# Kernel optimization log

Hardware: AMD Instinct MI355X
Metric: run time of the kernel (lower is better)

Reference implementation:

```python
import jax, jax.numpy as jnp
import numpy as np

N_NODES = 100000
N_EDGES = 1600000
IN_FEATS = 128
N_HIDDEN = 128
N_CLASSES = 47


def _glorot(key, shape):
    lim = float(np.sqrt(6.0 / (shape[0] + shape[1])))
    return jax.random.uniform(key, shape, jnp.float32, -lim, lim)


def setup_inputs() -> dict:
    key = jax.random.key(0)
    ks = jax.random.split(key, 9)
    x = jax.random.normal(ks[0], (N_NODES, IN_FEATS), jnp.float32)
    src = jax.random.randint(ks[1], (N_EDGES,), 0, N_NODES, jnp.int32)
    dst = jax.random.randint(ks[2], (N_EDGES,), 0, N_NODES, jnp.int32)
    return {
        "x": x,
        "W_self_0": _glorot(ks[3], (IN_FEATS, N_HIDDEN)),
        "W_neigh_0": _glorot(ks[4], (IN_FEATS, N_HIDDEN)),
        "W_self_1": _glorot(ks[5], (N_HIDDEN, N_HIDDEN)),
        "W_neigh_1": _glorot(ks[6], (N_HIDDEN, N_HIDDEN)),
        "W_self_2": _glorot(ks[7], (N_HIDDEN, N_CLASSES)),
        "W_neigh_2": _glorot(ks[8], (N_HIDDEN, N_CLASSES)),
        "src": src,
        "dst": dst,
    }


def _sage_layer(h, src, dst, W_self, W_neigh):
    # mean aggregation of in-neighbor features (DGL SAGEConv 'mean', no bias)
    neigh_sum = jax.ops.segment_sum(h[src], dst, num_segments=N_NODES)  # [N, d]
    deg = jax.ops.segment_sum(jnp.ones((src.shape[0],), h.dtype), dst,
                              num_segments=N_NODES)  # [N]
    h_neigh = neigh_sum / jnp.maximum(deg, 1.0)[:, None]
    return h @ W_self + h_neigh @ W_neigh


def reference(x, W_self_0, W_neigh_0, W_self_1, W_neigh_1, W_self_2, W_neigh_2,
              src, dst):
    h = _sage_layer(x, src, dst, W_self_0, W_neigh_0)
    h = jax.nn.relu(h)  # dropout is identity in eval/reference mode
    h = _sage_layer(h, src, dst, W_self_1, W_neigh_1)
    h = jax.nn.relu(h)
    h = _sage_layer(h, src, dst, W_self_2, W_neigh_2)
    return h
```

## Files before the change

### kernel.cpp

```cpp
#include <hip/hip_runtime.h>
#include <hip/hip_bf16.h>

#define NN 100000
#define NE 1600000
#define NBK 196

typedef __attribute__((ext_vector_type(8))) short bf16x8;
typedef __attribute__((ext_vector_type(4))) float f32x4;

__device__ __forceinline__ unsigned short f2bf(float x) {
    unsigned u = __float_as_uint(x);
    return (unsigned short)((u + 0x7fffu + ((u >> 16) & 1u)) >> 16);
}
__device__ __forceinline__ float bflo(unsigned v) { return __uint_as_float(v << 16); }
__device__ __forceinline__ float bfhi(unsigned v) { return __uint_as_float(v & 0xffff0000u); }

__global__ void cast_x(const float* __restrict__ x, unsigned short* __restrict__ h, int n) {
    int i = (blockIdx.x * blockDim.x + threadIdx.x) * 4;
    if (i >= n) return;
    float4 v = *(const float4*)(x + i);
    unsigned out0 = ((unsigned)f2bf(v.y) << 16) | f2bf(v.x);
    unsigned out1 = ((unsigned)f2bf(v.w) << 16) | f2bf(v.z);
    *(uint2*)(h + i) = make_uint2(out0, out1);
}

__global__ __launch_bounds__(256) void hist_buck(const int* __restrict__ dst, int* __restrict__ bhist) {
    __shared__ int h[NBK];
    int t = threadIdx.x;
    if (t < NBK) h[t] = 0;
    __syncthreads();
    int base = blockIdx.x * 4096;
#pragma unroll
    for (int i = 0; i < 16; ++i) {
        int e = base + t + i * 256;
        if (e < NE) atomicAdd(&h[dst[e] >> 9], 1);
    }
    __syncthreads();
    if (t < NBK && h[t]) atomicAdd(&bhist[t], h[t]);
}

__global__ void scan_buck(const int* __restrict__ bhist, int* __restrict__ bbase,
                          int* __restrict__ gcur, int* __restrict__ row_ptr) {
    __shared__ int s[256];
    int t = threadIdx.x;
    int v = (t < NBK) ? bhist[t] : 0;
    s[t] = v;
    __syncthreads();
    for (int off = 1; off < 256; off <<= 1) {
        int u = (t >= off) ? s[t - off] : 0;
        __syncthreads();
        s[t] += u;
        __syncthreads();
    }
    int ex = s[t] - v;
    if (t <= NBK) bbase[t] = ex;
    if (t < NBK) gcur[t * 16] = ex;
    if (t == 0) row_ptr[NN] = NE;
}

__global__ __launch_bounds__(256) void sort_scatter(const int* __restrict__ src,
                                                    const int* __restrict__ dst,
                                                    int* __restrict__ gcur,
                                                    unsigned* __restrict__ pairs) {
    __shared__ int bcnt[NBK], gbase[NBK], lcur[NBK];
    int t = threadIdx.x;
    if (t < NBK) { bcnt[t] = 0; lcur[t] = 0; }
    __syncthreads();
    int base = blockIdx.x * 4096;
#pragma unroll
    for (int i = 0; i < 16; ++i) {
        int e = base + t + i * 256;
        if (e < NE) atomicAdd(&bcnt[dst[e] >> 9], 1);
    }
    __syncthreads();
    if (t < NBK) gbase[t] = atomicAdd(&gcur[t * 16], bcnt[t]);
    __syncthreads();
#pragma unroll
    for (int i = 0; i < 16; ++i) {
        int e = base + t + i * 256;
        if (e < NE) {
            int d = dst[e];
            int b = d >> 9;
            int p = atomicAdd(&lcur[b], 1);
            pairs[gbase[b] + p] = ((unsigned)src[e] << 9) | (unsigned)(d & 511);
        }
    }
}

__global__ __launch_bounds__(512) void bucket_place(const unsigned* __restrict__ pairs,
                                                    const int* __restrict__ bbase,
                                                    int* __restrict__ row_ptr,
                                                    float* __restrict__ inv_deg,
                                                    int* __restrict__ csr) {
    __shared__ int hist[512], sc[512], cur[512];
    int b = blockIdx.x, t = threadIdx.x;
    hist[t] = 0;
    __syncthreads();
    int beg = bbase[b], end = bbase[b + 1];
    for (int i = beg + t; i < end; i += 512) atomicAdd(&hist[pairs[i] & 511u], 1);
    __syncthreads();
    int deg = hist[t];
    sc[t] = deg;
    __syncthreads();
    for (int off = 1; off < 512; off <<= 1) {
        int u = (t >= off) ? sc[t - off] : 0;
        __syncthreads();
        sc[t] += u;
        __syncthreads();
    }
    int ex = sc[t] - deg;
    int node = b * 512 + t;
    if (node < NN) {
        row_ptr[node] = beg + ex;
        inv_deg[node] = 1.0f / (float)max(deg, 1);
    }
    cur[t] = beg + ex;
    __syncthreads();
    for (int i = beg + t; i < end; i += 512) {
        unsigned p = pairs[i];
        int pos = atomicAdd(&cur[p & 511u], 1);
        csr[pos] = (int)(p >> 9);
    }
}

__global__ void pack_w(const float* __restrict__ Wself, const float* __restrict__ Wneigh,
                       unsigned short* __restrict__ wpack, int Ncols, int NF) {
    int idx = blockIdx.x * blockDim.x + threadIdx.x;
    int total = 8 * NF * 64 * 8;
    if (idx >= total) return;
    int j = idx & 7;
    int lane = (idx >> 3) & 63;
    int fid = idx >> 9;
    int nf = fid % NF;
    int kstep = fid / NF;
    int k = kstep * 32 + (lane >> 4) * 8 + j;
    int n = nf * 16 + (lane & 15);
    float v = 0.f;
    if (n < Ncols) v = (k < 128) ? Wself[k * Ncols + n] : Wneigh[(k - 128) * Ncols + n];
    wpack[idx] = f2bf(v);
}

__global__ void aggregate(const unsigned* __restrict__ h32, const int* __restrict__ csr,
                          const int* __restrict__ row_ptr, const float* __restrict__ inv_deg,
                          unsigned* __restrict__ agg32) {
    int lane = threadIdx.x & 63;
    int node = blockIdx.x * (blockDim.x >> 6) + (threadIdx.x >> 6);
    if (node >= NN) return;
    int beg = row_ptr[node], end = row_ptr[node + 1];
    float a0 = 0.f, a1 = 0.f, b0 = 0.f, b1 = 0.f;
    int e = beg;
    for (; e + 7 < end; e += 8) {
        int s0 = csr[e], s1 = csr[e + 1], s2 = csr[e + 2], s3 = csr[e + 3];
        int s4 = csr[e + 4], s5 = csr[e + 5], s6 = csr[e + 6], s7 = csr[e + 7];
        unsigned v0 = h32[s0 * 64 + lane];
        unsigned v1 = h32[s1 * 64 + lane];
        unsigned v2 = h32[s2 * 64 + lane];
        unsigned v3 = h32[s3 * 64 + lane];
        unsigned v4 = h32[s4 * 64 + lane];
        unsigned v5 = h32[s5 * 64 + lane];
        unsigned v6 = h32[s6 * 64 + lane];
        unsigned v7 = h32[s7 * 64 + lane];
        a0 += bflo(v0) + bflo(v1) + bflo(v2) + bflo(v3);
        a1 += bfhi(v0) + bfhi(v1) + bfhi(v2) + bfhi(v3);
        b0 += bflo(v4) + bflo(v5) + bflo(v6) + bflo(v7);
        b1 += bfhi(v4) + bfhi(v5) + bfhi(v6) + bfhi(v7);
    }
    for (; e + 3 < end; e += 4) {
        int s0 = csr[e], s1 = csr[e + 1], s2 = csr[e + 2], s3 = csr[e + 3];
        unsigned v0 = h32[s0 * 64 + lane];
        unsigned v1 = h32[s1 * 64 + lane];
        unsigned v2 = h32[s2 * 64 + lane];
        unsigned v3 = h32[s3 * 64 + lane];
        a0 += bflo(v0) + bflo(v1) + bflo(v2) + bflo(v3);
        a1 += bfhi(v0) + bfhi(v1) + bfhi(v2) + bfhi(v3);
    }
    for (; e < end; ++e) {
        unsigned v = h32[csr[e] * 64 + lane];
        a0 += bflo(v);
        a1 += bfhi(v);
    }
    a0 += b0; a1 += b1;
    float inv = inv_deg[node];
    a0 *= inv; a1 *= inv;
    agg32[node * 64 + lane] = ((unsigned)f2bf(a1) << 16) | f2bf(a0);
}

template <int NF, bool LAST>
__global__ __launch_bounds__(256) void gemm_k(const unsigned short* __restrict__ hA,
                                              const unsigned short* __restrict__ hAgg,
                                              const unsigned short* __restrict__ wpack,
                                              unsigned short* __restrict__ hOut,
                                              float* __restrict__ fOut) {
    int lane = threadIdx.x & 63;
    int wave = threadIdx.x >> 6;
    int aRow = blockIdx.x * 64 + wave * 16 + (lane & 15);
    int kgrp = (lane >> 4) * 8;

    f32x4 acc[NF];
#pragma unroll
    for (int f = 0; f < NF; ++f)
#pragma unroll
        for (int r = 0; r < 4; ++r) acc[f][r] = 0.f;

    bool inb = (aRow < NN);
#pragma unroll
    for (int half = 0; half < 2; ++half) {
        const unsigned short* A = half ? hAgg : hA;
#pragma unroll
        for (int ks = 0; ks < 4; ++ks) {
            bf16x8 afrag;
            if (inb) {
                afrag = *(const bf16x8*)(A + aRow * 128 + ks * 32 + kgrp);
            } else {
#pragma unroll
                for (int j = 0; j < 8; ++j) afrag[j] = 0;
            }
            int kstep = half * 4 + ks;
#pragma unroll
            for (int nf = 0; nf < NF; ++nf) {
                bf16x8 b = *(const bf16x8*)(wpack + (((kstep * NF + nf) * 64) + lane) * 8);
                acc[nf] = __builtin_amdgcn_mfma_f32_16x16x32_bf16(afrag, b, acc[nf], 0, 0, 0);
            }
        }
    }

    int col0 = lane & 15;
    int rBase = blockIdx.x * 64 + wave * 16 + (lane >> 4) * 4;
#pragma unroll
    for (int nf = 0; nf < NF; ++nf) {
        int col = nf * 16 + col0;
        if (LAST) {
            if (col < 47) {
#pragma unroll
                for (int r = 0; r < 4; ++r) {
                    int row = rBase + r;
                    if (row < NN) fOut[row * 47 + col] = acc[nf][r];
                }
            }
        } else {
#pragma unroll
            for (int r = 0; r < 4; ++r) {
                int row = rBase + r;
                if (row < NN) hOut[row * 128 + col] = f2bf(fmaxf(acc[nf][r], 0.f));
            }
        }
    }
}

static inline size_t alignup(size_t x) { return (x + 255) & ~(size_t)255; }

extern "C" void kernel_launch(void* const* d_in, const int* in_sizes, int n_in,
                              void* d_out, int out_size, void* d_ws, size_t ws_size,
                              hipStream_t stream) {
    const float* x   = (const float*)d_in[0];
    const float* Ws0 = (const float*)d_in[1];
    const float* Wn0 = (const float*)d_in[2];
    const float* Ws1 = (const float*)d_in[3];
    const float* Wn1 = (const float*)d_in[4];
    const float* Ws2 = (const float*)d_in[5];
    const float* Wn2 = (const float*)d_in[6];
    const int* src   = (const int*)d_in[7];
    const int* dst   = (const int*)d_in[8];
    float* out = (float*)d_out;

    char* w = (char*)d_ws;
    size_t off = 0;
    int* row_ptr   = (int*)(w + off);   off += alignup((NN + 1) * 4);
    int* bhist     = (int*)(w + off);   off += alignup(NBK * 4);
    int* bbase     = (int*)(w + off);   off += alignup((NBK + 1) * 4);
    int* gcur      = (int*)(w + off);   off += alignup((size_t)NBK * 16 * 4);
    float* inv_deg = (float*)(w + off); off += alignup(NN * 4);
    int* csr       = (int*)(w + off);   off += alignup((size_t)NE * 4);
    unsigned short* wp0 = (unsigned short*)(w + off); off += alignup(8 * 8 * 64 * 8 * 2);
    unsigned short* wp1 = (unsigned short*)(w + off); off += alignup(8 * 8 * 64 * 8 * 2);
    unsigned short* wp2 = (unsigned short*)(w + off); off += alignup(8 * 3 * 64 * 8 * 2);
    unsigned short* hA  = (unsigned short*)(w + off); off += alignup((size_t)NN * 128 * 2);
    unsigned short* hB  = (unsigned short*)(w + off); off += alignup((size_t)NN * 128 * 2);
    unsigned short* agg = (unsigned short*)(w + off); off += alignup((size_t)NN * 128 * 2);
    unsigned* pairs = (unsigned*)agg;

    hipMemsetAsync(bhist, 0, NBK * 4, stream);

    cast_x<<<dim3((NN * 128 / 4 + 255) / 256), dim3(256), 0, stream>>>(x, hA, NN * 128);
    hist_buck<<<dim3((NE + 4095) / 4096), dim3(256), 0, stream>>>(dst, bhist);
    scan_buck<<<dim3(1), dim3(256), 0, stream>>>(bhist, bbase, gcur, row_ptr);
    sort_scatter<<<dim3((NE + 4095) / 4096), dim3(256), 0, stream>>>(src, dst, gcur, pairs);
    bucket_place<<<dim3(NBK), dim3(512), 0, stream>>>(pairs, bbase, row_ptr, inv_deg, csr);

    pack_w<<<dim3((8 * 8 * 64 * 8 + 255) / 256), dim3(256), 0, stream>>>(Ws0, Wn0, wp0, 128, 8);
    pack_w<<<dim3((8 * 8 * 64 * 8 + 255) / 256), dim3(256), 0, stream>>>(Ws1, Wn1, wp1, 128, 8);
    pack_w<<<dim3((8 * 3 * 64 * 8 + 255) / 256), dim3(256), 0, stream>>>(Ws2, Wn2, wp2, 47, 3);

    const int gemmGrid = (NN + 63) / 64;

    aggregate<<<dim3(NN / 4), dim3(256), 0, stream>>>((const unsigned*)hA, csr, row_ptr, inv_deg, (unsigned*)agg);
    gemm_k<8, false><<<dim3(gemmGrid), dim3(256), 0, stream>>>(hA, agg, wp0, hB, nullptr);
    aggregate<<<dim3(NN / 4), dim3(256), 0, stream>>>((const unsigned*)hB, csr, row_ptr, inv_deg, (unsigned*)agg);
    gemm_k<8, false><<<dim3(gemmGrid), dim3(256), 0, stream>>>(hB, agg, wp1, hA, nullptr);
    aggregate<<<dim3(NN / 4), dim3(256), 0, stream>>>((const unsigned*)hA, csr, row_ptr, inv_deg, (unsigned*)agg);
    gemm_k<3, true><<<dim3(gemmGrid), dim3(256), 0, stream>>>(hA, agg, wp2, nullptr, out);
}
```

Before: 340.6 us.

## Fuse neighbor aggregation into GEMM via LDS-staged swizzled aggregate tile

```diff
diff --git a/kernel.cpp b/kernel.cpp
--- a/kernel.cpp
+++ b/kernel.cpp
@@ -119,7 +119,7 @@
     for (int i = beg + t; i < end; i += 512) {
         unsigned p = pairs[i];
         int pos = atomicAdd(&cur[p & 511u], 1);
-        csr[pos] = (int)(p >> 9);
+        csr[pos] = (int)(p >> 9) << 8;
     }
 }
 
@@ -140,108 +140,126 @@
     wpack[idx] = f2bf(v);
 }
 
-__global__ void aggregate(const unsigned* __restrict__ h32, const int* __restrict__ csr,
-                          const int* __restrict__ row_ptr, const float* __restrict__ inv_deg,
-                          unsigned* __restrict__ agg32) {
-    int lane = threadIdx.x & 63;
-    int node = blockIdx.x * (blockDim.x >> 6) + (threadIdx.x >> 6);
-    if (node >= NN) return;
-    int beg = row_ptr[node], end = row_ptr[node + 1];
-    float a0 = 0.f, a1 = 0.f, b0 = 0.f, b1 = 0.f;
-    int e = beg;
-    for (; e + 7 < end; e += 8) {
-        int s0 = csr[e], s1 = csr[e + 1], s2 = csr[e + 2], s3 = csr[e + 3];
-        int s4 = csr[e + 4], s5 = csr[e + 5], s6 = csr[e + 6], s7 = csr[e + 7];
-        unsigned v0 = h32[s0 * 64 + lane];
-        unsigned v1 = h32[s1 * 64 + lane];
-        unsigned v2 = h32[s2 * 64 + lane];
-        unsigned v3 = h32[s3 * 64 + lane];
-        unsigned v4 = h32[s4 * 64 + lane];
-        unsigned v5 = h32[s5 * 64 + lane];
-        unsigned v6 = h32[s6 * 64 + lane];
-        unsigned v7 = h32[s7 * 64 + lane];
-        a0 += bflo(v0) + bflo(v1) + bflo(v2) + bflo(v3);
-        a1 += bfhi(v0) + bfhi(v1) + bfhi(v2) + bfhi(v3);
-        b0 += bflo(v4) + bflo(v5) + bflo(v6) + bflo(v7);
-        b1 += bfhi(v4) + bfhi(v5) + bfhi(v6) + bfhi(v7);
-    }
-    for (; e + 3 < end; e += 4) {
-        int s0 = csr[e], s1 = csr[e + 1], s2 = csr[e + 2], s3 = csr[e + 3];
-        unsigned v0 = h32[s0 * 64 + lane];
-        unsigned v1 = h32[s1 * 64 + lane];
-        unsigned v2 = h32[s2 * 64 + lane];
-        unsigned v3 = h32[s3 * 64 + lane];
-        a0 += bflo(v0) + bflo(v1) + bflo(v2) + bflo(v3);
-        a1 += bfhi(v0) + bfhi(v1) + bfhi(v2) + bfhi(v3);
-    }
-    for (; e < end; ++e) {
-        unsigned v = h32[csr[e] * 64 + lane];
-        a0 += bflo(v);
-        a1 += bfhi(v);
-    }
-    a0 += b0; a1 += b1;
-    float inv = inv_deg[node];
-    a0 *= inv; a1 *= inv;
-    agg32[node * 64 + lane] = ((unsigned)f2bf(a1) << 16) | f2bf(a0);
-}
-
 template <int NF, bool LAST>
-__global__ __launch_bounds__(256) void gemm_k(const unsigned short* __restrict__ hA,
-                                              const unsigned short* __restrict__ hAgg,
-                                              const unsigned short* __restrict__ wpack,
-                                              unsigned short* __restrict__ hOut,
-                                              float* __restrict__ fOut) {
+__global__ __launch_bounds__(256) void sage_layer(const unsigned* __restrict__ h32,
+                                                  const int* __restrict__ csr,
+                                                  const int* __restrict__ row_ptr,
+                                                  const float* __restrict__ inv_deg,
+                                                  const unsigned short* __restrict__ wpack,
+                                                  unsigned short* __restrict__ hOut,
+                                                  float* __restrict__ fOut) {
+    __shared__ unsigned lds_agg[64 * 64];
     int lane = threadIdx.x & 63;
     int wave = threadIdx.x >> 6;
-    int aRow = blockIdx.x * 64 + wave * 16 + (lane & 15);
+    int base = blockIdx.x * 64;
+    const char* hb = (const char*)h32;
+    unsigned lane4 = (unsigned)lane * 4;
+
+    for (int i = 0; i < 16; ++i) {
+        int node = base + wave * 16 + i;
+        float a0 = 0.f, a1 = 0.f, b0 = 0.f, b1 = 0.f;
+        float inv = 0.f;
+        if (node < NN) {
+            int beg = row_ptr[node], end = row_ptr[node + 1];
+            inv = inv_deg[node];
+            int e = beg;
+            for (; e + 7 < end; e += 8) {
+                unsigned o0 = (unsigned)csr[e]     + lane4;
+                unsigned o1 = (unsigned)csr[e + 1] + lane4;
+                unsigned o2 = (unsigned)csr[e + 2] + lane4;
+                unsigned o3 = (unsigned)csr[e + 3] + lane4;
+                unsigned o4 = (unsigned)csr[e + 4] + lane4;
+                unsigned o5 = (unsigned)csr[e + 5] + lane4;
+                unsigned o6 = (unsigned)csr[e + 6] + lane4;
+                unsigned o7 = (unsigned)csr[e + 7] + lane4;
+                unsigned v0 = *(const unsigned*)(hb + o0);
+                unsigned v1 = *(const unsigned*)(hb + o1);
+                unsigned v2 = *(const unsigned*)(hb + o2);
+                unsigned v3 = *(const unsigned*)(hb + o3);
+                unsigned v4 = *(const unsigned*)(hb + o4);
+                unsigned v5 = *(const unsigned*)(hb + o5);
+                unsigned v6 = *(const unsigned*)(hb + o6);
+                unsigned v7 = *(const unsigned*)(hb + o7);
+                a0 += bflo(v0) + bflo(v1) + bflo(v2) + bflo(v3);
+                a1 += bfhi(v0) + bfhi(v1) + bfhi(v2) + bfhi(v3);
+                b0 += bflo(v4) + bflo(v5) + bflo(v6) + bflo(v7);
+                b1 += bfhi(v4) + bfhi(v5) + bfhi(v6) + bfhi(v7);
+            }
+            for (; e + 3 < end; e += 4) {
+                unsigned v0 = *(const unsigned*)(hb + (unsigned)csr[e]     + lane4);
+                unsigned v1 = *(const unsigned*)(hb + (unsigned)csr[e + 1] + lane4);
+                unsigned v2 = *(const unsigned*)(hb + (unsigned)csr[e + 2] + lane4);
+                unsigned v3 = *(const unsigned*)(hb + (unsigned)csr[e + 3] + lane4);
+                a0 += bflo(v0) + bflo(v1) + bflo(v2) + bflo(v3);
+                a1 += bfhi(v0) + bfhi(v1) + bfhi(v2) + bfhi(v3);
+            }
+            for (; e < end; ++e) {
+                unsigned v = *(const unsigned*)(hb + (unsigned)csr[e] + lane4);
+                a0 += bflo(v);
+                a1 += bfhi(v);
+            }
+            a0 = (a0 + b0) * inv;
+            a1 = (a1 + b1) * inv;
+        }
+        int r = wave * 16 + i;
+        lds_agg[r * 64 + (lane ^ ((r & 7) << 2))] = ((unsigned)f2bf(a1) << 16) | f2bf(a0);
+    }
+    __syncthreads();
+
+    int aRow = base + wave * 16 + (lane & 15);
     int kgrp = (lane >> 4) * 8;
+    int r = wave * 16 + (lane & 15);
+    int swz = (r & 7) << 2;
+    bool inb = (aRow < NN);
+    const unsigned short* hA = (const unsigned short*)h32;
 
     f32x4 acc[NF];
 #pragma unroll
     for (int f = 0; f < NF; ++f)
 #pragma unroll
-        for (int r = 0; r < 4; ++r) acc[f][r] = 0.f;
-
-    bool inb = (aRow < NN);
-#pragma unroll
-    for (int half = 0; half < 2; ++half) {
-        const unsigned short* A = half ? hAgg : hA;
-#pragma unroll
-        for (int ks = 0; ks < 4; ++ks) {
-            bf16x8 afrag;
-            if (inb) {
-                afrag = *(const bf16x8*)(A + aRow * 128 + ks * 32 + kgrp);
-            } else {
-#pragma unroll
-                for (int j = 0; j < 8; ++j) afrag[j] = 0;
-            }
-            int kstep = half * 4 + ks;
-#pragma unroll
-            for (int nf = 0; nf < NF; ++nf) {
-                bf16x8 b = *(const bf16x8*)(wpack + (((kstep * NF + nf) * 64) + lane) * 8);
-                acc[nf] = __builtin_amdgcn_mfma_f32_16x16x32_bf16(afrag, b, acc[nf], 0, 0, 0);
-            }
+        for (int q = 0; q < 4; ++q) acc[f][q] = 0.f;
+
+#pragma unroll
+    for (int ks = 0; ks < 4; ++ks) {
+        bf16x8 aSelf;
+        if (inb) {
+            aSelf = *(const bf16x8*)(hA + (size_t)aRow * 128 + ks * 32 + kgrp);
+        } else {
+#pragma unroll
+            for (int j = 0; j < 8; ++j) aSelf[j] = 0;
+        }
+#pragma unroll
+        for (int nf = 0; nf < NF; ++nf) {
+            bf16x8 b = *(const bf16x8*)(wpack + (((ks * NF + nf) * 64) + lane) * 8);
+            acc[nf] = __builtin_amdgcn_mfma_f32_16x16x32_bf16(aSelf, b, acc[nf], 0, 0, 0);
+        }
+        int d0 = ks * 16 + (lane >> 4) * 4;
+        bf16x8 aAgg = *(const bf16x8*)&lds_agg[r * 64 + (d0 ^ swz)];
+#pragma unroll
+        for (int nf = 0; nf < NF; ++nf) {
+            bf16x8 b = *(const bf16x8*)(wpack + ((((4 + ks) * NF + nf) * 64) + lane) * 8);
+            acc[nf] = __builtin_amdgcn_mfma_f32_16x16x32_bf16(aAgg, b, acc[nf], 0, 0, 0);
         }
     }
 
     int col0 = lane & 15;
-    int rBase = blockIdx.x * 64 + wave * 16 + (lane >> 4) * 4;
+    int rBase = base + wave * 16 + (lane >> 4) * 4;
 #pragma unroll
     for (int nf = 0; nf < NF; ++nf) {
         int col = nf * 16 + col0;
         if (LAST) {
             if (col < 47) {
 #pragma unroll
-                for (int r = 0; r < 4; ++r) {
-                    int row = rBase + r;
-                    if (row < NN) fOut[row * 47 + col] = acc[nf][r];
+                for (int q = 0; q < 4; ++q) {
+                    int row = rBase + q;
+                    if (row < NN) fOut[(size_t)row * 47 + col] = acc[nf][q];
                 }
             }
         } else {
 #pragma unroll
-            for (int r = 0; r < 4; ++r) {
-                int row = rBase + r;
-                if (row < NN) hOut[row * 128 + col] = f2bf(fmaxf(acc[nf][r], 0.f));
+            for (int q = 0; q < 4; ++q) {
+                int row = rBase + q;
+                if (row < NN) hOut[(size_t)row * 128 + col] = f2bf(fmaxf(acc[nf][q], 0.f));
             }
         }
     }
@@ -271,13 +289,12 @@
     int* gcur      = (int*)(w + off);   off += alignup((size_t)NBK * 16 * 4);
     float* inv_deg = (float*)(w + off); off += alignup(NN * 4);
     int* csr       = (int*)(w + off);   off += alignup((size_t)NE * 4);
+    unsigned* pairs = (unsigned*)(w + off); off += alignup((size_t)NE * 4);
     unsigned short* wp0 = (unsigned short*)(w + off); off += alignup(8 * 8 * 64 * 8 * 2);
     unsigned short* wp1 = (unsigned short*)(w + off); off += alignup(8 * 8 * 64 * 8 * 2);
     unsigned short* wp2 = (unsigned short*)(w + off); off += alignup(8 * 3 * 64 * 8 * 2);
     unsigned short* hA  = (unsigned short*)(w + off); off += alignup((size_t)NN * 128 * 2);
     unsigned short* hB  = (unsigned short*)(w + off); off += alignup((size_t)NN * 128 * 2);
-    unsigned short* agg = (unsigned short*)(w + off); off += alignup((size_t)NN * 128 * 2);
-    unsigned* pairs = (unsigned*)agg;
 
     hipMemsetAsync(bhist, 0, NBK * 4, stream);
 
@@ -291,12 +308,11 @@
     pack_w<<<dim3((8 * 8 * 64 * 8 + 255) / 256), dim3(256), 0, stream>>>(Ws1, Wn1, wp1, 128, 8);
     pack_w<<<dim3((8 * 3 * 64 * 8 + 255) / 256), dim3(256), 0, stream>>>(Ws2, Wn2, wp2, 47, 3);
 
-    const int gemmGrid = (NN + 63) / 64;
-
-    aggregate<<<dim3(NN / 4), dim3(256), 0, stream>>>((const unsigned*)hA, csr, row_ptr, inv_deg, (unsigned*)agg);
-    gemm_k<8, false><<<dim3(gemmGrid), dim3(256), 0, stream>>>(hA, agg, wp0, hB, nullptr);
-    aggregate<<<dim3(NN / 4), dim3(256), 0, stream>>>((const unsigned*)hB, csr, row_ptr, inv_deg, (unsigned*)agg);
-    gemm_k<8, false><<<dim3(gemmGrid), dim3(256), 0, stream>>>(hB, agg, wp1, hA, nullptr);
-    aggregate<<<dim3(NN / 4), dim3(256), 0, stream>>>((const unsigned*)hA, csr, row_ptr, inv_deg, (unsigned*)agg);
-    gemm_k<3, true><<<dim3(gemmGrid), dim3(256), 0, stream>>>(hA, agg, wp2, nullptr, out);
-}
+    const int grid = (NN + 63) / 64;
+    sage_layer<8, false><<<dim3(grid), dim3(256), 0, stream>>>(
+        (const unsigned*)hA, csr, row_ptr, inv_deg, wp0, hB, nullptr);
+    sage_layer<8, false><<<dim3(grid), dim3(256), 0, stream>>>(
+        (const unsigned*)hB, csr, row_ptr, inv_deg, wp1, hA, nullptr);
+    sage_layer<3, true><<<dim3(grid), dim3(256), 0, stream>>>(
+        (const unsigned*)hA, csr, row_ptr, inv_deg, wp2, nullptr, out);
+}
```

After: 388.2 us. +14.0%, slower.

## Reorder last layer to transform-then-aggregate and vectorize neighbor gathers

Applied to the files above, without the earlier changes.

```diff
diff --git a/kernel.cpp b/kernel.cpp
--- a/kernel.cpp
+++ b/kernel.cpp
@@ -14,6 +14,12 @@
 }
 __device__ __forceinline__ float bflo(unsigned v) { return __uint_as_float(v << 16); }
 __device__ __forceinline__ float bfhi(unsigned v) { return __uint_as_float(v & 0xffff0000u); }
+
+#define ACC8(v) do { \
+    acc[0] += bflo((v).x); acc[1] += bfhi((v).x); \
+    acc[2] += bflo((v).y); acc[3] += bfhi((v).y); \
+    acc[4] += bflo((v).z); acc[5] += bfhi((v).z); \
+    acc[6] += bflo((v).w); acc[7] += bfhi((v).w); } while (0)
 
 __global__ void cast_x(const float* __restrict__ x, unsigned short* __restrict__ h, int n) {
     int i = (blockIdx.x * blockDim.x + threadIdx.x) * 4;
@@ -119,7 +125,7 @@
     for (int i = beg + t; i < end; i += 512) {
         unsigned p = pairs[i];
         int pos = atomicAdd(&cur[p & 511u], 1);
-        csr[pos] = (int)(p >> 9);
+        csr[pos] = (int)(p >> 9) << 8;
     }
 }
 
@@ -140,57 +146,122 @@
     wpack[idx] = f2bf(v);
 }
 
-__global__ void aggregate(const unsigned* __restrict__ h32, const int* __restrict__ csr,
-                          const int* __restrict__ row_ptr, const float* __restrict__ inv_deg,
-                          unsigned* __restrict__ agg32) {
+__global__ __launch_bounds__(256) void aggregate(const unsigned* __restrict__ h32,
+                                                 const int* __restrict__ csr,
+                                                 const int* __restrict__ row_ptr,
+                                                 const float* __restrict__ inv_deg,
+                                                 unsigned* __restrict__ agg32) {
     int lane = threadIdx.x & 63;
-    int node = blockIdx.x * (blockDim.x >> 6) + (threadIdx.x >> 6);
+    int wave = threadIdx.x >> 6;
+    int node = blockIdx.x * 4 + wave;
     if (node >= NN) return;
+    int g = lane >> 4;
+    unsigned l16 = (unsigned)(lane & 15) * 16;
+    const char* hb = (const char*)h32;
     int beg = row_ptr[node], end = row_ptr[node + 1];
-    float a0 = 0.f, a1 = 0.f, b0 = 0.f, b1 = 0.f;
+    float acc[8];
+#pragma unroll
+    for (int j = 0; j < 8; ++j) acc[j] = 0.f;
+
     int e = beg;
+    for (; e + 15 < end; e += 16) {
+        int c0 = csr[e + g];
+        int c1 = csr[e + 4 + g];
+        int c2 = csr[e + 8 + g];
+        int c3 = csr[e + 12 + g];
+        uint4 v0 = *(const uint4*)(hb + (unsigned)c0 + l16);
+        uint4 v1 = *(const uint4*)(hb + (unsigned)c1 + l16);
+        uint4 v2 = *(const uint4*)(hb + (unsigned)c2 + l16);
+        uint4 v3 = *(const uint4*)(hb + (unsigned)c3 + l16);
+        ACC8(v0); ACC8(v1); ACC8(v2); ACC8(v3);
+    }
+    for (; e + 3 < end; e += 4) {
+        int c = csr[e + g];
+        uint4 v = *(const uint4*)(hb + (unsigned)c + l16);
+        ACC8(v);
+    }
+    int rem = end - e;
+    if (g < rem) {
+        int c = csr[e + g];
+        uint4 v = *(const uint4*)(hb + (unsigned)c + l16);
+        ACC8(v);
+    }
+
+#pragma unroll
+    for (int j = 0; j < 8; ++j) {
+        acc[j] += __shfl_xor(acc[j], 16, 64);
+        acc[j] += __shfl_xor(acc[j], 32, 64);
+    }
+    float inv = inv_deg[node];
+    if (lane < 16) {
+        unsigned d0 = ((unsigned)f2bf(acc[1] * inv) << 16) | f2bf(acc[0] * inv);
+        unsigned d1 = ((unsigned)f2bf(acc[3] * inv) << 16) | f2bf(acc[2] * inv);
+        unsigned d2 = ((unsigned)f2bf(acc[5] * inv) << 16) | f2bf(acc[4] * inv);
+        unsigned d3 = ((unsigned)f2bf(acc[7] * inv) << 16) | f2bf(acc[6] * inv);
+        *(uint4*)((char*)agg32 + (size_t)node * 256 + l16) = make_uint4(d0, d1, d2, d3);
+    }
+}
+
+__global__ __launch_bounds__(256) void agg_out(const unsigned* __restrict__ g32,
+                                               const int* __restrict__ csr,
+                                               const int* __restrict__ row_ptr,
+                                               const float* __restrict__ inv_deg,
+                                               float* __restrict__ out) {
+    int lane = threadIdx.x & 63;
+    int wave = threadIdx.x >> 6;
+    int node = blockIdx.x * 4 + wave;
+    if (node >= NN) return;
+    int g = lane >> 3;
+    int l = lane & 7;
+    unsigned l16 = (unsigned)l * 16;
+    const char* gb = (const char*)g32;
+    int beg = row_ptr[node], end = row_ptr[node + 1];
+    float acc[8];
+#pragma unroll
+    for (int j = 0; j < 8; ++j) acc[j] = 0.f;
+
+    int e = beg;
+    for (; e + 15 < end; e += 16) {
+        int c0 = csr[e + g];
+        int c1 = csr[e + 8 + g];
+        uint4 v0 = *(const uint4*)(gb + ((unsigned)c0 >> 1) + l16);
+        uint4 v1 = *(const uint4*)(gb + ((unsigned)c1 >> 1) + l16);
+        ACC8(v0); ACC8(v1);
+    }
     for (; e + 7 < end; e += 8) {
-        int s0 = csr[e], s1 = csr[e + 1], s2 = csr[e + 2], s3 = csr[e + 3];
-        int s4 = csr[e + 4], s5 = csr[e + 5], s6 = csr[e + 6], s7 = csr[e + 7];
-        unsigned v0 = h32[s0 * 64 + lane];
-        unsigned v1 = h32[s1 * 64 + lane];
-        unsigned v2 = h32[s2 * 64 + lane];
-        unsigned v3 = h32[s3 * 64 + lane];
-        unsigned v4 = h32[s4 * 64 + lane];
-        unsigned v5 = h32[s5 * 64 + lane];
-        unsigned v6 = h32[s6 * 64 + lane];
-        unsigned v7 = h32[s7 * 64 + lane];
-        a0 += bflo(v0) + bflo(v1) + bflo(v2) + bflo(v3);
-        a1 += bfhi(v0) + bfhi(v1) + bfhi(v2) + bfhi(v3);
-        b0 += bflo(v4) + bflo(v5) + bflo(v6) + bflo(v7);
-        b1 += bfhi(v4) + bfhi(v5) + bfhi(v6) + bfhi(v7);
-    }
-    for (; e + 3 < end; e += 4) {
-        int s0 = csr[e], s1 = csr[e + 1], s2 = csr[e + 2], s3 = csr[e + 3];
-        unsigned v0 = h32[s0 * 64 + lane];
-        unsigned v1 = h32[s1 * 64 + lane];
-        unsigned v2 = h32[s2 * 64 + lane];
-        unsigned v3 = h32[s3 * 64 + lane];
-        a0 += bflo(v0) + bflo(v1) + bflo(v2) + bflo(v3);
-        a1 += bfhi(v0) + bfhi(v1) + bfhi(v2) + bfhi(v3);
-    }
-    for (; e < end; ++e) {
-        unsigned v = h32[csr[e] * 64 + lane];
-        a0 += bflo(v);
-        a1 += bfhi(v);
-    }
-    a0 += b0; a1 += b1;
+        int c = csr[e + g];
+        uint4 v = *(const uint4*)(gb + ((unsigned)c >> 1) + l16);
+        ACC8(v);
+    }
+    int rem = end - e;
+    if (g < rem) {
+        int c = csr[e + g];
+        uint4 v = *(const uint4*)(gb + ((unsigned)c >> 1) + l16);
+        ACC8(v);
+    }
+
+#pragma unroll
+    for (int j = 0; j < 8; ++j) {
+        acc[j] += __shfl_xor(acc[j], 8, 64);
+        acc[j] += __shfl_xor(acc[j], 16, 64);
+        acc[j] += __shfl_xor(acc[j], 32, 64);
+    }
     float inv = inv_deg[node];
-    a0 *= inv; a1 *= inv;
-    agg32[node * 64 + lane] = ((unsigned)f2bf(a1) << 16) | f2bf(a0);
-}
-
-template <int NF, bool LAST>
+    if (lane < 8) {
+        float* orow = out + (size_t)node * 47;
+#pragma unroll
+        for (int j = 0; j < 8; ++j) {
+            int f = l * 8 + j;
+            if (f < 47) orow[f] += acc[j] * inv;
+        }
+    }
+}
+
+template <int NF>
 __global__ __launch_bounds__(256) void gemm_k(const unsigned short* __restrict__ hA,
                                               const unsigned short* __restrict__ hAgg,
                                               const unsigned short* __restrict__ wpack,
-                                              unsigned short* __restrict__ hOut,
-                                              float* __restrict__ fOut) {
+                                              unsigned short* __restrict__ hOut) {
     int lane = threadIdx.x & 63;
     int wave = threadIdx.x >> 6;
     int aRow = blockIdx.x * 64 + wave * 16 + (lane & 15);
@@ -200,7 +271,7 @@
 #pragma unroll
     for (int f = 0; f < NF; ++f)
 #pragma unroll
-        for (int r = 0; r < 4; ++r) acc[f][r] = 0.f;
+        for (int q = 0; q < 4; ++q) acc[f][q] = 0.f;
 
     bool inb = (aRow < NN);
 #pragma unroll
@@ -210,7 +281,7 @@
         for (int ks = 0; ks < 4; ++ks) {
             bf16x8 afrag;
             if (inb) {
-                afrag = *(const bf16x8*)(A + aRow * 128 + ks * 32 + kgrp);
+                afrag = *(const bf16x8*)(A + (size_t)aRow * 128 + ks * 32 + kgrp);
             } else {
 #pragma unroll
                 for (int j = 0; j < 8; ++j) afrag[j] = 0;
@@ -229,19 +300,59 @@
 #pragma unroll
     for (int nf = 0; nf < NF; ++nf) {
         int col = nf * 16 + col0;
-        if (LAST) {
-            if (col < 47) {
-#pragma unroll
-                for (int r = 0; r < 4; ++r) {
-                    int row = rBase + r;
-                    if (row < NN) fOut[row * 47 + col] = acc[nf][r];
-                }
-            }
+#pragma unroll
+        for (int q = 0; q < 4; ++q) {
+            int row = rBase + q;
+            if (row < NN) hOut[(size_t)row * 128 + col] = f2bf(fmaxf(acc[nf][q], 0.f));
+        }
+    }
+}
+
+__global__ __launch_bounds__(256) void gemm_last(const unsigned short* __restrict__ hA,
+                                                 const unsigned short* __restrict__ wpack,
+                                                 unsigned short* __restrict__ g64,
+                                                 float* __restrict__ out) {
+    int lane = threadIdx.x & 63;
+    int wave = threadIdx.x >> 6;
+    int aRow = blockIdx.x * 64 + wave * 16 + (lane & 15);
+    int kgrp = (lane >> 4) * 8;
+
+    f32x4 accS[3], accG[3];
+#pragma unroll
+    for (int f = 0; f < 3; ++f)
+#pragma unroll
+        for (int q = 0; q < 4; ++q) { accS[f][q] = 0.f; accG[f][q] = 0.f; }
+
+    bool inb = (aRow < NN);
+#pragma unroll
+    for (int ks = 0; ks < 4; ++ks) {
+        bf16x8 afrag;
+        if (inb) {
+            afrag = *(const bf16x8*)(hA + (size_t)aRow * 128 + ks * 32 + kgrp);
         } else {
 #pragma unroll
-            for (int r = 0; r < 4; ++r) {
-                int row = rBase + r;
-                if (row < NN) hOut[row * 128 + col] = f2bf(fmaxf(acc[nf][r], 0.f));
+            for (int j = 0; j < 8; ++j) afrag[j] = 0;
+        }
+#pragma unroll
+        for (int nf = 0; nf < 3; ++nf) {
+            bf16x8 bS = *(const bf16x8*)(wpack + (((ks * 3 + nf) * 64) + lane) * 8);
+            accS[nf] = __builtin_amdgcn_mfma_f32_16x16x32_bf16(afrag, bS, accS[nf], 0, 0, 0);
+            bf16x8 bG = *(const bf16x8*)(wpack + ((((4 + ks) * 3 + nf) * 64) + lane) * 8);
+            accG[nf] = __builtin_amdgcn_mfma_f32_16x16x32_bf16(afrag, bG, accG[nf], 0, 0, 0);
+        }
+    }
+
+    int col0 = lane & 15;
+    int rBase = blockIdx.x * 64 + wave * 16 + (lane >> 4) * 4;
+#pragma unroll
+    for (int nf = 0; nf < 3; ++nf) {
+        int col = nf * 16 + col0;
+#pragma unroll
+        for (int q = 0; q < 4; ++q) {
+            int row = rBase + q;
+            if (row < NN) {
+                if (col < 47) out[(size_t)row * 47 + col] = accS[nf][q];
+                g64[(size_t)row * 64 + col] = f2bf(accG[nf][q]);
             }
         }
     }
@@ -271,13 +382,14 @@
     int* gcur      = (int*)(w + off);   off += alignup((size_t)NBK * 16 * 4);
     float* inv_deg = (float*)(w + off); off += alignup(NN * 4);
     int* csr       = (int*)(w + off);   off += alignup((size_t)NE * 4);
+    unsigned* pairs = (unsigned*)(w + off); off += alignup((size_t)NE * 4);
     unsigned short* wp0 = (unsigned short*)(w + off); off += alignup(8 * 8 * 64 * 8 * 2);
     unsigned short* wp1 = (unsigned short*)(w + off); off += alignup(8 * 8 * 64 * 8 * 2);
     unsigned short* wp2 = (unsigned short*)(w + off); off += alignup(8 * 3 * 64 * 8 * 2);
     unsigned short* hA  = (unsigned short*)(w + off); off += alignup((size_t)NN * 128 * 2);
     unsigned short* hB  = (unsigned short*)(w + off); off += alignup((size_t)NN * 128 * 2);
     unsigned short* agg = (unsigned short*)(w + off); off += alignup((size_t)NN * 128 * 2);
-    unsigned* pairs = (unsigned*)agg;
+    unsigned short* g64 = agg;
 
     hipMemsetAsync(bhist, 0, NBK * 4, stream);
 
@@ -291,12 +403,13 @@
     pack_w<<<dim3((8 * 8 * 64 * 8 + 255) / 256), dim3(256), 0, stream>>>(Ws1, Wn1, wp1, 128, 8);
     pack_w<<<dim3((8 * 3 * 64 * 8 + 255) / 256), dim3(256), 0, stream>>>(Ws2, Wn2, wp2, 47, 3);
 
+    const int aggGrid  = (NN + 3) / 4;
     const int gemmGrid = (NN + 63) / 64;
 
-    aggregate<<<dim3(NN / 4), dim3(256), 0, stream>>>((const unsigned*)hA, csr, row_ptr, inv_deg, (unsigned*)agg);
-    gemm_k<8, false><<<dim3(gemmGrid), dim3(256), 0, stream>>>(hA, agg, wp0, hB, nullptr);
-    aggregate<<<dim3(NN / 4), dim3(256), 0, stream>>>((const unsigned*)hB, csr, row_ptr, inv_deg, (unsigned*)agg);
-    gemm_k<8, false><<<dim3(gemmGrid), dim3(256), 0, stream>>>(hB, agg, wp1, hA, nullptr);
-    aggregate<<<dim3(NN / 4), dim3(256), 0, stream>>>((const unsigned*)hA, csr, row_ptr, inv_deg, (unsigned*)agg);
-    gemm_k<3, true><<<dim3(gemmGrid), dim3(256), 0, stream>>>(hA, agg, wp2, nullptr, out);
-}
+    aggregate<<<dim3(aggGrid), dim3(256), 0, stream>>>((const unsigned*)hA, csr, row_ptr, inv_deg, (unsigned*)agg);
+    gemm_k<8><<<dim3(gemmGrid), dim3(256), 0, stream>>>(hA, agg, wp0, hB);
+    aggregate<<<dim3(aggGrid), dim3(256), 0, stream>>>((const unsigned*)hB, csr, row_ptr, inv_deg, (unsigned*)agg);
+    gemm_k<8><<<dim3(gemmGrid), dim3(256), 0, stream>>>(hB, agg, wp1, hA);
+    gemm_last<<<dim3(gemmGrid), dim3(256), 0, stream>>>(hA, wp2, g64, out);
+    agg_out<<<dim3(aggGrid), dim3(256), 0, stream>>>((const unsigned*)g64, csr, row_ptr, inv_deg, out);
+}
```

Result: no change. 343.0 us (+0.7%).

## Restructure aggregation: two nodes per wave with 16-byte row gathers

Applied to the files above, without the earlier changes.

```diff
diff --git a/kernel.cpp b/kernel.cpp
--- a/kernel.cpp
+++ b/kernel.cpp
@@ -14,6 +14,31 @@
 }
 __device__ __forceinline__ float bflo(unsigned v) { return __uint_as_float(v << 16); }
 __device__ __forceinline__ float bfhi(unsigned v) { return __uint_as_float(v & 0xffff0000u); }
+
+#define ACCV(A, v) do { \
+    A[0] += bflo((v).x); A[1] += bfhi((v).x); \
+    A[2] += bflo((v).y); A[3] += bfhi((v).y); \
+    A[4] += bflo((v).z); A[5] += bfhi((v).z); \
+    A[6] += bflo((v).w); A[7] += bfhi((v).w); } while (0)
+
+#define DRAIN(A, e, end) do { \
+    for (; e + 15 < end; e += 16) { \
+        int c0 = csr[e + g], c1 = csr[e + 4 + g], c2 = csr[e + 8 + g], c3 = csr[e + 12 + g]; \
+        uint4 w0 = *(const uint4*)(hb + (unsigned)c0 + l16); \
+        uint4 w1 = *(const uint4*)(hb + (unsigned)c1 + l16); \
+        uint4 w2 = *(const uint4*)(hb + (unsigned)c2 + l16); \
+        uint4 w3 = *(const uint4*)(hb + (unsigned)c3 + l16); \
+        ACCV(A, w0); ACCV(A, w1); ACCV(A, w2); ACCV(A, w3); } \
+    for (; e + 3 < end; e += 4) { \
+        int c = csr[e + g]; \
+        uint4 w = *(const uint4*)(hb + (unsigned)c + l16); \
+        ACCV(A, w); } \
+    { int rem = end - e; \
+      if (g < rem) { \
+        int c = csr[e + g]; \
+        uint4 w = *(const uint4*)(hb + (unsigned)c + l16); \
+        ACCV(A, w); } } \
+} while (0)
 
 __global__ void cast_x(const float* __restrict__ x, unsigned short* __restrict__ h, int n) {
     int i = (blockIdx.x * blockDim.x + threadIdx.x) * 4;
@@ -119,70 +144,93 @@
     for (int i = beg + t; i < end; i += 512) {
         unsigned p = pairs[i];
         int pos = atomicAdd(&cur[p & 511u], 1);
-        csr[pos] = (int)(p >> 9);
-    }
-}
-
-__global__ void pack_w(const float* __restrict__ Wself, const float* __restrict__ Wneigh,
-                       unsigned short* __restrict__ wpack, int Ncols, int NF) {
+        csr[pos] = (int)(p >> 9) << 8;
+    }
+}
+
+__global__ void pack_w_all(const float* __restrict__ Ws0, const float* __restrict__ Wn0,
+                           const float* __restrict__ Ws1, const float* __restrict__ Wn1,
+                           const float* __restrict__ Ws2, const float* __restrict__ Wn2,
+                           unsigned short* __restrict__ wp0, unsigned short* __restrict__ wp1,
+                           unsigned short* __restrict__ wp2) {
     int idx = blockIdx.x * blockDim.x + threadIdx.x;
-    int total = 8 * NF * 64 * 8;
-    if (idx >= total) return;
-    int j = idx & 7;
-    int lane = (idx >> 3) & 63;
-    int fid = idx >> 9;
+    const float *Ws, *Wn;
+    unsigned short* wp;
+    int Ncols, NF, local;
+    if (idx < 32768)       { Ws = Ws0; Wn = Wn0; wp = wp0; Ncols = 128; NF = 8; local = idx; }
+    else if (idx < 65536)  { Ws = Ws1; Wn = Wn1; wp = wp1; Ncols = 128; NF = 8; local = idx - 32768; }
+    else if (idx < 77824)  { Ws = Ws2; Wn = Wn2; wp = wp2; Ncols = 47;  NF = 3; local = idx - 65536; }
+    else return;
+    int j = local & 7;
+    int lane = (local >> 3) & 63;
+    int fid = local >> 9;
     int nf = fid % NF;
     int kstep = fid / NF;
     int k = kstep * 32 + (lane >> 4) * 8 + j;
     int n = nf * 16 + (lane & 15);
     float v = 0.f;
-    if (n < Ncols) v = (k < 128) ? Wself[k * Ncols + n] : Wneigh[(k - 128) * Ncols + n];
-    wpack[idx] = f2bf(v);
-}
-
-__global__ void aggregate(const unsigned* __restrict__ h32, const int* __restrict__ csr,
-                          const int* __restrict__ row_ptr, const float* __restrict__ inv_deg,
-                          unsigned* __restrict__ agg32) {
+    if (n < Ncols) v = (k < 128) ? Ws[k * Ncols + n] : Wn[(k - 128) * Ncols + n];
+    wp[local] = f2bf(v);
+}
+
+__global__ __launch_bounds__(256) void aggregate(const unsigned* __restrict__ h32,
+                                                 const int* __restrict__ csr,
+                                                 const int* __restrict__ row_ptr,
+                                                 const float* __restrict__ inv_deg,
+                                                 unsigned* __restrict__ agg32) {
     int lane = threadIdx.x & 63;
-    int node = blockIdx.x * (blockDim.x >> 6) + (threadIdx.x >> 6);
-    if (node >= NN) return;
-    int beg = row_ptr[node], end = row_ptr[node + 1];
-    float a0 = 0.f, a1 = 0.f, b0 = 0.f, b1 = 0.f;
-    int e = beg;
-    for (; e + 7 < end; e += 8) {
-        int s0 = csr[e], s1 = csr[e + 1], s2 = csr[e + 2], s3 = csr[e + 3];
-        int s4 = csr[e + 4], s5 = csr[e + 5], s6 = csr[e + 6], s7 = csr[e + 7];
-        unsigned v0 = h32[s0 * 64 + lane];
-        unsigned v1 = h32[s1 * 64 + lane];
-        unsigned v2 = h32[s2 * 64 + lane];
-        unsigned v3 = h32[s3 * 64 + lane];
-        unsigned v4 = h32[s4 * 64 + lane];
-        unsigned v5 = h32[s5 * 64 + lane];
-        unsigned v6 = h32[s6 * 64 + lane];
-        unsigned v7 = h32[s7 * 64 + lane];
-        a0 += bflo(v0) + bflo(v1) + bflo(v2) + bflo(v3);
-        a1 += bfhi(v0) + bfhi(v1) + bfhi(v2) + bfhi(v3);
-        b0 += bflo(v4) + bflo(v5) + bflo(v6) + bflo(v7);
-        b1 += bfhi(v4) + bfhi(v5) + bfhi(v6) + bfhi(v7);
-    }
-    for (; e + 3 < end; e += 4) {
-        int s0 = csr[e], s1 = csr[e + 1], s2 = csr[e + 2], s3 = csr[e + 3];
-        unsigned v0 = h32[s0 * 64 + lane];
-        unsigned v1 = h32[s1 * 64 + lane];
-        unsigned v2 = h32[s2 * 64 + lane];
-        unsigned v3 = h32[s3 * 64 + lane];
-        a0 += bflo(v0) + bflo(v1) + bflo(v2) + bflo(v3);
-        a1 += bfhi(v0) + bfhi(v1) + bfhi(v2) + bfhi(v3);
-    }
-    for (; e < end; ++e) {
-        unsigned v = h32[csr[e] * 64 + lane];
-        a0 += bflo(v);
-        a1 += bfhi(v);
-    }
-    a0 += b0; a1 += b1;
-    float inv = inv_deg[node];
-    a0 *= inv; a1 *= inv;
-    agg32[node * 64 + lane] = ((unsigned)f2bf(a1) << 16) | f2bf(a0);
+    int wave = threadIdx.x >> 6;
+    int n0 = (blockIdx.x * 4 + wave) * 2;
+    if (n0 >= NN) return;
+    int g = lane >> 4;
+    unsigned l16 = (unsigned)(lane & 15) * 16;
+    const char* hb = (const char*)h32;
+    int b0  = row_ptr[n0];
+    int m0  = row_ptr[n0 + 1];
+    int e1e = row_ptr[n0 + 2];
+
+    float a[8], b[8];
+#pragma unroll
+    for (int j = 0; j < 8; ++j) { a[j] = 0.f; b[j] = 0.f; }
+
+    int e0 = b0, e1 = m0;
+    while (e0 + 15 < m0 && e1 + 15 < e1e) {
+        int c00 = csr[e0 + g], c01 = csr[e0 + 4 + g], c02 = csr[e0 + 8 + g], c03 = csr[e0 + 12 + g];
+        int c10 = csr[e1 + g], c11 = csr[e1 + 4 + g], c12 = csr[e1 + 8 + g], c13 = csr[e1 + 12 + g];
+        uint4 v00 = *(const uint4*)(hb + (unsigned)c00 + l16);
+        uint4 v01 = *(const uint4*)(hb + (unsigned)c01 + l16);
+        uint4 v02 = *(const uint4*)(hb + (unsigned)c02 + l16);
+        uint4 v03 = *(const uint4*)(hb + (unsigned)c03 + l16);
+        uint4 v10 = *(const uint4*)(hb + (unsigned)c10 + l16);
+        uint4 v11 = *(const uint4*)(hb + (unsigned)c11 + l16);
+        uint4 v12 = *(const uint4*)(hb + (unsigned)c12 + l16);
+        uint4 v13 = *(const uint4*)(hb + (unsigned)c13 + l16);
+        ACCV(a, v00); ACCV(a, v01); ACCV(a, v02); ACCV(a, v03);
+        ACCV(b, v10); ACCV(b, v11); ACCV(b, v12); ACCV(b, v13);
+        e0 += 16; e1 += 16;
+    }
+    DRAIN(a, e0, m0);
+    DRAIN(b, e1, e1e);
+
+#pragma unroll
+    for (int j = 0; j < 8; ++j) {
+        a[j] += __shfl_xor(a[j], 16, 64);
+        a[j] += __shfl_xor(a[j], 32, 64);
+        b[j] += __shfl_xor(b[j], 16, 64);
+        b[j] += __shfl_xor(b[j], 32, 64);
+    }
+    float inv = inv_deg[n0 + ((lane >> 4) & 1)];
+    if (lane < 32) {
+        float r[8];
+#pragma unroll
+        for (int j = 0; j < 8; ++j) r[j] = ((lane < 16) ? a[j] : b[j]) * inv;
+        unsigned d0 = ((unsigned)f2bf(r[1]) << 16) | f2bf(r[0]);
+        unsigned d1 = ((unsigned)f2bf(r[3]) << 16) | f2bf(r[2]);
+        unsigned d2 = ((unsigned)f2bf(r[5]) << 16) | f2bf(r[4]);
+        unsigned d3 = ((unsigned)f2bf(r[7]) << 16) | f2bf(r[6]);
+        int node = n0 + (lane >> 4);
+        *(uint4*)((char*)agg32 + (size_t)node * 256 + l16) = make_uint4(d0, d1, d2, d3);
+    }
 }
 
 template <int NF, bool LAST>
@@ -200,7 +248,7 @@
 #pragma unroll
     for (int f = 0; f < NF; ++f)
 #pragma unroll
-        for (int r = 0; r < 4; ++r) acc[f][r] = 0.f;
+        for (int q = 0; q < 4; ++q) acc[f][q] = 0.f;
 
     bool inb = (aRow < NN);
 #pragma unroll
@@ -210,7 +258,7 @@
         for (int ks = 0; ks < 4; ++ks) {
             bf16x8 afrag;
             if (inb) {
-                afrag = *(const bf16x8*)(A + aRow * 128 + ks * 32 + kgrp);
+                afrag = *(const bf16x8*)(A + (size_t)aRow * 128 + ks * 32 + kgrp);
             } else {
 #pragma unroll
                 for (int j = 0; j < 8; ++j) afrag[j] = 0;
@@ -232,16 +280,16 @@
         if (LAST) {
             if (col < 47) {
 #pragma unroll
-                for (int r = 0; r < 4; ++r) {
-                    int row = rBase + r;
-                    if (row < NN) fOut[row * 47 + col] = acc[nf][r];
+                for (int q = 0; q < 4; ++q) {
+                    int row = rBase + q;
+                    if (row < NN) fOut[(size_t)row * 47 + col] = acc[nf][q];
                 }
             }
         } else {
 #pragma unroll
-            for (int r = 0; r < 4; ++r) {
-                int row = rBase + r;
-                if (row < NN) hOut[row * 128 + col] = f2bf(fmaxf(acc[nf][r], 0.f));
+            for (int q = 0; q < 4; ++q) {
+                int row = rBase + q;
+                if (row < NN) hOut[(size_t)row * 128 + col] = f2bf(fmaxf(acc[nf][q], 0.f));
             }
         }
     }
@@ -271,13 +319,13 @@
     int* gcur      = (int*)(w + off);   off += alignup((size_t)NBK * 16 * 4);
     float* inv_deg = (float*)(w + off); off += alignup(NN * 4);
     int* csr       = (int*)(w + off);   off += alignup((size_t)NE * 4);
+    unsigned* pairs = (unsigned*)(w + off); off += alignup((size_t)NE * 4);
     unsigned short* wp0 = (unsigned short*)(w + off); off += alignup(8 * 8 * 64 * 8 * 2);
     unsigned short* wp1 = (unsigned short*)(w + off); off += alignup(8 * 8 * 64 * 8 * 2);
     unsigned short* wp2 = (unsigned short*)(w + off); off += alignup(8 * 3 * 64 * 8 * 2);
     unsigned short* hA  = (unsigned short*)(w + off); off += alignup((size_t)NN * 128 * 2);
     unsigned short* hB  = (unsigned short*)(w + off); off += alignup((size_t)NN * 128 * 2);
     unsigned short* agg = (unsigned short*)(w + off); off += alignup((size_t)NN * 128 * 2);
-    unsigned* pairs = (unsigned*)agg;
 
     hipMemsetAsync(bhist, 0, NBK * 4, stream);
 
@@ -287,16 +335,16 @@
     sort_scatter<<<dim3((NE + 4095) / 4096), dim3(256), 0, stream>>>(src, dst, gcur, pairs);
     bucket_place<<<dim3(NBK), dim3(512), 0, stream>>>(pairs, bbase, row_ptr, inv_deg, csr);
 
-    pack_w<<<dim3((8 * 8 * 64 * 8 + 255) / 256), dim3(256), 0, stream>>>(Ws0, Wn0, wp0, 128, 8);
-    pack_w<<<dim3((8 * 8 * 64 * 8 + 255) / 256), dim3(256), 0, stream>>>(Ws1, Wn1, wp1, 128, 8);
-    pack_w<<<dim3((8 * 3 * 64 * 8 + 255) / 256), dim3(256), 0, stream>>>(Ws2, Wn2, wp2, 47, 3);
-
+    pack_w_all<<<dim3((77824 + 255) / 256), dim3(256), 0, stream>>>(
+        Ws0, Wn0, Ws1, Wn1, Ws2, Wn2, wp0, wp1, wp2);
+
+    const int aggGrid  = (NN / 2 + 3) / 4;
     const int gemmGrid = (NN + 63) / 64;
 
-    aggregate<<<dim3(NN / 4), dim3(256), 0, stream>>>((const unsigned*)hA, csr, row_ptr, inv_deg, (unsigned*)agg);
+    aggregate<<<dim3(aggGrid), dim3(256), 0, stream>>>((const unsigned*)hA, csr, row_ptr, inv_deg, (unsigned*)agg);
     gemm_k<8, false><<<dim3(gemmGrid), dim3(256), 0, stream>>>(hA, agg, wp0, hB, nullptr);
-    aggregate<<<dim3(NN / 4), dim3(256), 0, stream>>>((const unsigned*)hB, csr, row_ptr, inv_deg, (unsigned*)agg);
+    aggregate<<<dim3(aggGrid), dim3(256), 0, stream>>>((const unsigned*)hB, csr, row_ptr, inv_deg, (unsigned*)agg);
     gemm_k<8, false><<<dim3(gemmGrid), dim3(256), 0, stream>>>(hB, agg, wp1, hA, nullptr);
-    aggregate<<<dim3(NN / 4), dim3(256), 0, stream>>>((const unsigned*)hA, csr, row_ptr, inv_deg, (unsigned*)agg);
+    aggregate<<<dim3(aggGrid), dim3(256), 0, stream>>>((const unsigned*)hA, csr, row_ptr, inv_deg, (unsigned*)agg);
     gemm_k<3, true><<<dim3(gemmGrid), dim3(256), 0, stream>>>(hA, agg, wp2, nullptr, out);
 }
```

Result: slower. 388.6 us (+14.1%).
